# Kernel tuning notes

Hardware: AMD Instinct MI355X
Metric: run time of the kernel (lower is better)

The kernel has to match this reference:

```python
import jax, jax.numpy as jnp
import numpy as np

B, D, NT, NZ = 16384, 64, 128, 2048


def setup_inputs() -> dict:
    key = jax.random.key(0)
    ks = jax.random.split(key, 5)
    return {
        "t": jax.random.uniform(ks[0], (1,), dtype=jnp.float32),
        "z": jax.random.normal(ks[1], (B, D), dtype=jnp.float32),
        "logp_z": jnp.zeros((B, 1), jnp.float32),
        "centres_z": jax.random.normal(ks[2], (NZ, D), dtype=jnp.float32),
        "log_sigmas_z": jnp.zeros((NZ,), jnp.float32),
        "centres_t": jax.random.normal(ks[3], (NT, 1), dtype=jnp.float32),
        "log_sigmas_t": jnp.zeros((NT,), jnp.float32),
        "W": 0.01 * jax.random.normal(ks[4], (D, NT, NZ + 1), dtype=jnp.float32),
    }


def _gauss(r):
    return jnp.exp(-r * r)


def _forward(t, z, centres_z, log_sigmas_z, centres_t, log_sigmas_t, W):
    # time RBF features Phi_t: (NT,)
    r_t = jnp.abs(t.reshape(1, 1) - centres_t.reshape(1, -1)) / jnp.exp(log_sigmas_t)
    phi_t = _gauss(r_t).reshape(-1)
    W_t = jnp.einsum('dij,i->dj', W, phi_t)  # (D, NZ+1)
    Wz, bias = W_t[:, :-1], W_t[:, -1]       # bias comes from the appended ones column
    # z RBF features via squared-distance identity (avoids [B,NZ,D] blowup)
    sq = (jnp.sum(z * z, axis=1, keepdims=True)
          + jnp.sum(centres_z * centres_z, axis=1)[None, :]
          - 2.0 * z @ centres_z.T)
    sq = jnp.maximum(sq, 0.0)                 # (B, NZ) squared distances
    inv_s2 = jnp.exp(-2.0 * log_sigmas_z)     # 1/sigma_j^2, (NZ,)
    phi_z = jnp.exp(-sq * inv_s2)             # gaussian(||z-c_j||/s_j), (B, NZ)
    dz_dt = phi_z @ Wz.T + bias               # (B, D)
    # exact Jacobian trace for gaussian basis:
    #   d phi_j / d z_i = -2 * phi_j * (z_i - c_{j,i}) / s_j^2
    #   tr(J)_b = sum_j phi_{b,j} * inv_s2_j * (-2) * (sum_i Wz[i,j] z_{b,i} - sum_i Wz[i,j] c_{j,i})
    q = jnp.einsum('dj,jd->j', Wz, centres_z)  # (NZ,)
    trace = -2.0 * jnp.sum(phi_z * inv_s2 * (z @ Wz - q), axis=1)  # (B,)
    dlogp_z_dt = -trace[:, None]               # (B, 1)
    return dz_dt, dlogp_z_dt


def reference(t, z, logp_z, centres_z, log_sigmas_z, centres_t, log_sigmas_t, W):
    return _forward(t, z, centres_z, log_sigmas_z, centres_t, log_sigmas_t, W)
```

## Files before the change

kernel.cpp:

```cpp
#include <hip/hip_runtime.h>
#include <math.h>

typedef unsigned int uint;
typedef unsigned short ushort;
typedef __attribute__((ext_vector_type(8))) short short8;
typedef __attribute__((ext_vector_type(4))) float f32x4;

#define BB  16384
#define DD  64
#define NT_ 128
#define NZ_ 2048
#define NJ_ 2049

#define BIAS_OFF 0
#define Q_OFF    64
#define CC_OFF   2112
#define INV_OFF  4160
#define ZB_OFF   6208
#define CZB_OFF  530496
#define WZTB_OFF 596032
#define WZB_OFF  661568

__device__ __forceinline__ ushort f2b(float x) {
  uint u = __float_as_uint(x);
  uint r = (u + 0x7FFFu + ((u >> 16) & 1u)) >> 16;
  return (ushort)r;
}
__device__ __forceinline__ float b2f(ushort h) {
  return __uint_as_float(((uint)h) << 16);
}

__global__ __launch_bounds__(256) void k_wt(
    const float* __restrict__ t, const float* __restrict__ ct,
    const float* __restrict__ lst, const float* __restrict__ W,
    ushort* __restrict__ wzb, float* __restrict__ bias)
{
  __shared__ float ph[NT_];
  int tx = threadIdx.x;
  float t0 = t[0];
  if (tx < NT_) {
    float r = fabsf(t0 - ct[tx]) * __expf(-lst[tx]);
    ph[tx] = __expf(-r * r);
  }
  __syncthreads();
  int d = blockIdx.y;
  int j = blockIdx.x * 256 + tx;
  if (j >= NJ_) return;
  const float* Wp = W + (size_t)d * NT_ * NJ_ + j;
  float acc = 0.f;
#pragma unroll 16
  for (int i = 0; i < NT_; ++i) acc += Wp[(size_t)i * NJ_] * ph[i];
  if (j < NZ_) wzb[d * NZ_ + j] = f2b(acc);
  else         bias[d] = acc;
}

__global__ __launch_bounds__(256) void k_prep(
    const float* __restrict__ cz, const float* __restrict__ lsz,
    const ushort* __restrict__ wzb,
    float* __restrict__ q, float* __restrict__ cc, float* __restrict__ inv,
    ushort* __restrict__ czb, ushort* __restrict__ wztb)
{
  __shared__ ushort wt[64][72];
  int tid = threadIdx.x;
  int cb0 = blockIdx.x * 64;
#pragma unroll
  for (int k = 0; k < 2; ++k) {
    int f = k * 256 + tid;
    int d = f >> 3, s = f & 7;
    *(short8*)&wt[d][s * 8] = *(const short8*)(wzb + (size_t)d * NZ_ + cb0 + s * 8);
  }
  __syncthreads();
  int c_l = tid >> 2, part = tid & 3;
  int c = cb0 + c_l;
  float qa = 0.f, ca = 0.f;
  ushort czl[16];
  const float4* cz4 = (const float4*)(cz + (size_t)c * DD + part * 16);
#pragma unroll
  for (int x = 0; x < 4; ++x) {
    float4 v = cz4[x];
    float va[4] = {v.x, v.y, v.z, v.w};
#pragma unroll
    for (int k = 0; k < 4; ++k) {
      int d = part * 16 + x * 4 + k;
      ca += va[k] * va[k];
      qa += b2f(wt[d][c_l]) * va[k];
      czl[x * 4 + k] = f2b(va[k]);
    }
  }
  {
    short8 o0, o1;
#pragma unroll
    for (int k = 0; k < 8; ++k) { o0[k] = (short)czl[k]; o1[k] = (short)czl[8 + k]; }
    *(short8*)(czb + (size_t)c * DD + part * 16)     = o0;
    *(short8*)(czb + (size_t)c * DD + part * 16 + 8) = o1;
  }
  {
    short8 o0, o1;
#pragma unroll
    for (int k = 0; k < 8; ++k) {
      o0[k] = (short)wt[part * 16 + k][c_l];
      o1[k] = (short)wt[part * 16 + 8 + k][c_l];
    }
    *(short8*)(wztb + (size_t)c * DD + part * 16)     = o0;
    *(short8*)(wztb + (size_t)c * DD + part * 16 + 8) = o1;
  }
  qa += __shfl_xor(qa, 1); qa += __shfl_xor(qa, 2);
  ca += __shfl_xor(ca, 1); ca += __shfl_xor(ca, 2);
  if (part == 0) {
    q[c]  = qa;
    cc[c] = ca;
    inv[c] = __expf(-2.f * lsz[c]);
  }
}

__global__ __launch_bounds__(256) void k_zb(
    const float* __restrict__ z, ushort* __restrict__ zb)
{
  int f = blockIdx.x * 256 + threadIdx.x;
  const float4* z4 = (const float4*)z;
  float4 v0 = z4[f * 2], v1 = z4[f * 2 + 1];
  short8 o;
  o[0] = (short)f2b(v0.x); o[1] = (short)f2b(v0.y);
  o[2] = (short)f2b(v0.z); o[3] = (short)f2b(v0.w);
  o[4] = (short)f2b(v1.x); o[5] = (short)f2b(v1.y);
  o[6] = (short)f2b(v1.z); o[7] = (short)f2b(v1.w);
  *(short8*)(zb + (size_t)f * 8) = o;
}

#define KC 32

__global__ __launch_bounds__(512) void k_fused(
    const ushort* __restrict__ zb,
    const ushort* __restrict__ czb,
    const ushort* __restrict__ wztb,
    const ushort* __restrict__ wzb,
    const float* __restrict__ qg, const float* __restrict__ ccg,
    const float* __restrict__ invg, const float* __restrict__ bias,
    float* __restrict__ out)
{
  __shared__ float qs[NZ_], ccs[NZ_], invs[NZ_];
  __shared__ ushort phs[8][2][16][40];
  __shared__ float eps[64][68];
  __shared__ float dlr[4][64];

  int tid  = threadIdx.x;
  int wv   = tid >> 6, lane = tid & 63;
  int lrow = lane & 15, quad = lane >> 4;
  int ws = wv >> 1;
  int h  = wv & 1;
  int b0 = blockIdx.x * 64;

#pragma unroll
  for (int k = 0; k < 4; ++k) {
    int idx = k * 512 + tid;
    qs[idx] = qg[idx]; ccs[idx] = ccg[idx]; invs[idx] = invg[idx];
  }

  short8 a[2][2];
#pragma unroll
  for (int mt = 0; mt < 2; ++mt) {
    const ushort* zr = zb + (size_t)(b0 + h * 32 + mt * 16 + lrow) * DD;
    a[mt][0] = *(const short8*)(zr + quad * 8);
    a[mt][1] = *(const short8*)(zr + 32 + quad * 8);
  }
  float zzr[2][4];
#pragma unroll
  for (int mt = 0; mt < 2; ++mt) {
    float p = 0.f;
#pragma unroll
    for (int k = 0; k < 8; ++k) {
      float v0 = b2f((ushort)a[mt][0][k]), v1 = b2f((ushort)a[mt][1][k]);
      p += v0 * v0 + v1 * v1;
    }
    p += __shfl_xor(p, 16);
    p += __shfl_xor(p, 32);
#pragma unroll
    for (int i = 0; i < 4; ++i) zzr[mt][i] = __shfl(p, quad * 4 + i);
  }
  __syncthreads();

  f32x4 acc[2][4];
#pragma unroll
  for (int mt = 0; mt < 2; ++mt)
#pragma unroll
    for (int nt = 0; nt < 4; ++nt) acc[mt][nt] = (f32x4){0.f, 0.f, 0.f, 0.f};
  float dl[2][4] = {{0.f}};

  const f32x4 zero = (f32x4){0.f, 0.f, 0.f, 0.f};
  int cbase = ws * 512;
  for (int cc0 = 0; cc0 < 512; cc0 += KC) {
    int c0 = cbase + cc0;
#pragma unroll
    for (int nt = 0; nt < 2; ++nt) {
      const ushort* cr = czb  + (size_t)(c0 + nt * 16 + lrow) * DD;
      const ushort* wr = wztb + (size_t)(c0 + nt * 16 + lrow) * DD;
      short8 bc0 = *(const short8*)(cr + quad * 8);
      short8 bc1 = *(const short8*)(cr + 32 + quad * 8);
      short8 bw0 = *(const short8*)(wr + quad * 8);
      short8 bw1 = *(const short8*)(wr + 32 + quad * 8);
      int cl = nt * 16 + lrow, cg = c0 + cl;
      float ccv = ccs[cg], iv = invs[cg], qv = qs[cg];
#pragma unroll
      for (int mt = 0; mt < 2; ++mt) {
        f32x4 d1 = __builtin_amdgcn_mfma_f32_16x16x32_bf16(a[mt][0], bc0, zero, 0, 0, 0);
        d1       = __builtin_amdgcn_mfma_f32_16x16x32_bf16(a[mt][1], bc1, d1,   0, 0, 0);
        f32x4 d2 = __builtin_amdgcn_mfma_f32_16x16x32_bf16(a[mt][0], bw0, zero, 0, 0, 0);
        d2       = __builtin_amdgcn_mfma_f32_16x16x32_bf16(a[mt][1], bw1, d2,   0, 0, 0);
#pragma unroll
        for (int i = 0; i < 4; ++i) {
          float s = zzr[mt][i] + ccv - 2.f * d1[i];
          s = fmaxf(s, 0.f);
          float p = __expf(-s * iv);
          dl[mt][i] += p * iv * (d2[i] - qv);
          phs[wv][mt][quad * 4 + i][cl] = f2b(p);
        }
      }
    }
    short8 ap0 = *(const short8*)&phs[wv][0][lrow][quad * 8];
    short8 ap1 = *(const short8*)&phs[wv][1][lrow][quad * 8];
#pragma unroll
    for (int nt = 0; nt < 4; ++nt) {
      short8 bb = *(const short8*)(wzb + (size_t)(nt * 16 + lrow) * NZ_ + c0 + quad * 8);
      acc[0][nt] = __builtin_amdgcn_mfma_f32_16x16x32_bf16(ap0, bb, acc[0][nt], 0, 0, 0);
      acc[1][nt] = __builtin_amdgcn_mfma_f32_16x16x32_bf16(ap1, bb, acc[1][nt], 0, 0, 0);
    }
  }

#pragma unroll
  for (int mt = 0; mt < 2; ++mt)
#pragma unroll
    for (int i = 0; i < 4; ++i) {
      float v = dl[mt][i];
      v += __shfl_xor(v, 1);
      v += __shfl_xor(v, 2);
      v += __shfl_xor(v, 4);
      v += __shfl_xor(v, 8);
      if (lrow == 0) dlr[ws][h * 32 + mt * 16 + quad * 4 + i] = v;
    }

  for (int s = 0; s < 4; ++s) {
    __syncthreads();
    if (ws == s) {
#pragma unroll
      for (int mt = 0; mt < 2; ++mt)
#pragma unroll
        for (int nt = 0; nt < 4; ++nt)
#pragma unroll
          for (int i = 0; i < 4; ++i) {
            int r = h * 32 + mt * 16 + quad * 4 + i;
            int d = nt * 16 + lrow;
            if (s == 0) eps[r][d] = acc[mt][nt][i];
            else        eps[r][d] += acc[mt][nt][i];
          }
    }
  }
  __syncthreads();

  {
    int r = tid >> 3, d0 = (tid & 7) * 8;
    float4 e0 = *(const float4*)&eps[r][d0];
    float4 e1 = *(const float4*)&eps[r][d0 + 4];
    float4 bv0 = *(const float4*)&bias[d0];
    float4 bv1 = *(const float4*)&bias[d0 + 4];
    float4 o0, o1;
    o0.x = e0.x + bv0.x; o0.y = e0.y + bv0.y; o0.z = e0.z + bv0.z; o0.w = e0.w + bv0.w;
    o1.x = e1.x + bv1.x; o1.y = e1.y + bv1.y; o1.z = e1.z + bv1.z; o1.w = e1.w + bv1.w;
    *(float4*)&out[(size_t)(b0 + r) * DD + d0]     = o0;
    *(float4*)&out[(size_t)(b0 + r) * DD + d0 + 4] = o1;
  }
  if (tid < 64) {
    float s = dlr[0][tid] + dlr[1][tid] + dlr[2][tid] + dlr[3][tid];
    out[(size_t)BB * DD + b0 + tid] = 2.f * s;
  }
}

extern "C" void kernel_launch(void* const* d_in, const int* in_sizes, int n_in,
                              void* d_out, int out_size, void* d_ws, size_t ws_size,
                              hipStream_t stream)
{
  const float* t   = (const float*)d_in[0];
  const float* z   = (const float*)d_in[1];
  const float* cz  = (const float*)d_in[3];
  const float* lsz = (const float*)d_in[4];
  const float* ct  = (const float*)d_in[5];
  const float* lst = (const float*)d_in[6];
  const float* W   = (const float*)d_in[7];
  float* out = (float*)d_out;
  float* ws  = (float*)d_ws;

  float*  bias = ws + BIAS_OFF;
  float*  q    = ws + Q_OFF;
  float*  cc   = ws + CC_OFF;
  float*  inv  = ws + INV_OFF;
  ushort* zbp  = (ushort*)(ws + ZB_OFF);
  ushort* czb  = (ushort*)(ws + CZB_OFF);
  ushort* wztb = (ushort*)(ws + WZTB_OFF);
  ushort* wzb  = (ushort*)(ws + WZB_OFF);

  k_wt<<<dim3(9, 64), 256, 0, stream>>>(t, ct, lst, W, wzb, bias);
  k_prep<<<dim3(32), 256, 0, stream>>>(cz, lsz, wzb, q, cc, inv, czb, wztb);
  k_zb<<<dim3(512), 256, 0, stream>>>(z, zbp);
  k_fused<<<dim3(BB / 64), 512, 0, stream>>>(zbp, czb, wztb, wzb, q, cc, inv, bias, out);
}
```

Measured before the change: 165.0 us.

## Split W contraction over time-RBF chunks and shrink fused kernel LDS footprint

The W-by-phi_t contraction is split into four chunks of 32 time centres across a third grid dimension. Each chunk writes float partials, and the prep kernel sums them and also produces the bf16 Wz, its transpose and the bias. The goal is more parallelism when streaming the large W tensor. In the fused kernel the per-centre q/cc/inv tables are no longer staged in shared memory and are read from global memory instead. The phi and epilogue buffers now share one aliased LDS region, with launch bounds requesting more resident blocks. This trades extra partial-sum traffic and global scalar loads for higher occupancy.

```diff
diff --git a/kernel.cpp b/kernel.cpp
--- a/kernel.cpp
+++ b/kernel.cpp
@@ -20,6 +20,7 @@
 #define CZB_OFF  530496
 #define WZTB_OFF 596032
 #define WZB_OFF  661568
+#define PART_OFF 727104
 
 __device__ __forceinline__ ushort f2b(float x) {
   uint u = __float_as_uint(x);
@@ -30,60 +31,70 @@
   return __uint_as_float(((uint)h) << 16);
 }
 
-__global__ __launch_bounds__(256) void k_wt(
+__global__ __launch_bounds__(256) void k_wt1(
     const float* __restrict__ t, const float* __restrict__ ct,
     const float* __restrict__ lst, const float* __restrict__ W,
-    ushort* __restrict__ wzb, float* __restrict__ bias)
-{
-  __shared__ float ph[NT_];
+    float* __restrict__ part)
+{
+  __shared__ float ph[32];
   int tx = threadIdx.x;
-  float t0 = t[0];
-  if (tx < NT_) {
-    float r = fabsf(t0 - ct[tx]) * __expf(-lst[tx]);
+  int d  = blockIdx.y;
+  int ic = blockIdx.z;
+  if (tx < 32) {
+    int i = ic * 32 + tx;
+    float r = fabsf(t[0] - ct[i]) * __expf(-lst[i]);
     ph[tx] = __expf(-r * r);
   }
   __syncthreads();
-  int d = blockIdx.y;
   int j = blockIdx.x * 256 + tx;
   if (j >= NJ_) return;
-  const float* Wp = W + (size_t)d * NT_ * NJ_ + j;
+  const float* Wp = W + (size_t)d * NT_ * NJ_ + (size_t)(ic * 32) * NJ_ + j;
   float acc = 0.f;
-#pragma unroll 16
-  for (int i = 0; i < NT_; ++i) acc += Wp[(size_t)i * NJ_] * ph[i];
-  if (j < NZ_) wzb[d * NZ_ + j] = f2b(acc);
-  else         bias[d] = acc;
+#pragma unroll
+  for (int k = 0; k < 32; ++k) acc += Wp[(size_t)k * NJ_] * ph[k];
+  part[((size_t)ic * 64 + d) * NJ_ + j] = acc;
 }
 
 __global__ __launch_bounds__(256) void k_prep(
-    const float* __restrict__ cz, const float* __restrict__ lsz,
-    const ushort* __restrict__ wzb,
+    const float* __restrict__ part, const float* __restrict__ cz,
+    const float* __restrict__ lsz,
     float* __restrict__ q, float* __restrict__ cc, float* __restrict__ inv,
-    ushort* __restrict__ czb, ushort* __restrict__ wztb)
-{
-  __shared__ ushort wt[64][72];
+    float* __restrict__ bias,
+    ushort* __restrict__ wzb, ushort* __restrict__ czb, ushort* __restrict__ wztb)
+{
+  __shared__ float wtf[64][65];
   int tid = threadIdx.x;
   int cb0 = blockIdx.x * 64;
 #pragma unroll
-  for (int k = 0; k < 2; ++k) {
+  for (int k = 0; k < 16; ++k) {
     int f = k * 256 + tid;
-    int d = f >> 3, s = f & 7;
-    *(short8*)&wt[d][s * 8] = *(const short8*)(wzb + (size_t)d * NZ_ + cb0 + s * 8);
+    int d = f >> 6, c = f & 63;
+    size_t idx = (size_t)d * NJ_ + cb0 + c;
+    float s = part[idx] + part[(size_t)64 * NJ_ + idx]
+            + part[(size_t)128 * NJ_ + idx] + part[(size_t)192 * NJ_ + idx];
+    wtf[d][c] = s;
+    wzb[(size_t)d * NZ_ + cb0 + c] = f2b(s);
+  }
+  if (blockIdx.x == 0 && tid < 64) {
+    size_t idx = (size_t)tid * NJ_ + 2048;
+    bias[tid] = part[idx] + part[(size_t)64 * NJ_ + idx]
+              + part[(size_t)128 * NJ_ + idx] + part[(size_t)192 * NJ_ + idx];
   }
   __syncthreads();
-  int c_l = tid >> 2, part = tid & 3;
+  int c_l = tid >> 2, part4 = tid & 3;
   int c = cb0 + c_l;
   float qa = 0.f, ca = 0.f;
   ushort czl[16];
-  const float4* cz4 = (const float4*)(cz + (size_t)c * DD + part * 16);
+  const float4* cz4 = (const float4*)(cz + (size_t)c * DD + part4 * 16);
 #pragma unroll
   for (int x = 0; x < 4; ++x) {
     float4 v = cz4[x];
     float va[4] = {v.x, v.y, v.z, v.w};
 #pragma unroll
     for (int k = 0; k < 4; ++k) {
-      int d = part * 16 + x * 4 + k;
+      int d = part4 * 16 + x * 4 + k;
       ca += va[k] * va[k];
-      qa += b2f(wt[d][c_l]) * va[k];
+      qa += wtf[d][c_l] * va[k];
       czl[x * 4 + k] = f2b(va[k]);
     }
   }
@@ -91,22 +102,22 @@
     short8 o0, o1;
 #pragma unroll
     for (int k = 0; k < 8; ++k) { o0[k] = (short)czl[k]; o1[k] = (short)czl[8 + k]; }
-    *(short8*)(czb + (size_t)c * DD + part * 16)     = o0;
-    *(short8*)(czb + (size_t)c * DD + part * 16 + 8) = o1;
+    *(short8*)(czb + (size_t)c * DD + part4 * 16)     = o0;
+    *(short8*)(czb + (size_t)c * DD + part4 * 16 + 8) = o1;
   }
   {
     short8 o0, o1;
 #pragma unroll
     for (int k = 0; k < 8; ++k) {
-      o0[k] = (short)wt[part * 16 + k][c_l];
-      o1[k] = (short)wt[part * 16 + 8 + k][c_l];
-    }
-    *(short8*)(wztb + (size_t)c * DD + part * 16)     = o0;
-    *(short8*)(wztb + (size_t)c * DD + part * 16 + 8) = o1;
+      o0[k] = (short)f2b(wtf[part4 * 16 + k][c_l]);
+      o1[k] = (short)f2b(wtf[part4 * 16 + 8 + k][c_l]);
+    }
+    *(short8*)(wztb + (size_t)c * DD + part4 * 16)     = o0;
+    *(short8*)(wztb + (size_t)c * DD + part4 * 16 + 8) = o1;
   }
   qa += __shfl_xor(qa, 1); qa += __shfl_xor(qa, 2);
   ca += __shfl_xor(ca, 1); ca += __shfl_xor(ca, 2);
-  if (part == 0) {
+  if (part4 == 0) {
     q[c]  = qa;
     cc[c] = ca;
     inv[c] = __expf(-2.f * lsz[c]);
@@ -128,8 +139,9 @@
 }
 
 #define KC 32
-
-__global__ __launch_bounds__(512) void k_fused(
+#define PH_LD 40
+
+__global__ __launch_bounds__(512, 6) void k_fused(
     const ushort* __restrict__ zb,
     const ushort* __restrict__ czb,
     const ushort* __restrict__ wztb,
@@ -138,10 +150,10 @@
     const float* __restrict__ invg, const float* __restrict__ bias,
     float* __restrict__ out)
 {
-  __shared__ float qs[NZ_], ccs[NZ_], invs[NZ_];
-  __shared__ ushort phs[8][2][16][40];
-  __shared__ float eps[64][68];
+  __shared__ char smem[20480];
   __shared__ float dlr[4][64];
+  ushort* phs = (ushort*)smem;
+  float*  eps = (float*)smem;
 
   int tid  = threadIdx.x;
   int wv   = tid >> 6, lane = tid & 63;
@@ -150,12 +162,6 @@
   int h  = wv & 1;
   int b0 = blockIdx.x * 64;
 
-#pragma unroll
-  for (int k = 0; k < 4; ++k) {
-    int idx = k * 512 + tid;
-    qs[idx] = qg[idx]; ccs[idx] = ccg[idx]; invs[idx] = invg[idx];
-  }
-
   short8 a[2][2];
 #pragma unroll
   for (int mt = 0; mt < 2; ++mt) {
@@ -177,7 +183,6 @@
 #pragma unroll
     for (int i = 0; i < 4; ++i) zzr[mt][i] = __shfl(p, quad * 4 + i);
   }
-  __syncthreads();
 
   f32x4 acc[2][4];
 #pragma unroll
@@ -188,18 +193,19 @@
 
   const f32x4 zero = (f32x4){0.f, 0.f, 0.f, 0.f};
   int cbase = ws * 512;
+  int pbase = (wv * 2) * 16 * PH_LD;
   for (int cc0 = 0; cc0 < 512; cc0 += KC) {
     int c0 = cbase + cc0;
 #pragma unroll
     for (int nt = 0; nt < 2; ++nt) {
-      const ushort* cr = czb  + (size_t)(c0 + nt * 16 + lrow) * DD;
-      const ushort* wr = wztb + (size_t)(c0 + nt * 16 + lrow) * DD;
+      int cl = nt * 16 + lrow, cg = c0 + cl;
+      const ushort* cr = czb  + (size_t)cg * DD;
+      const ushort* wr = wztb + (size_t)cg * DD;
       short8 bc0 = *(const short8*)(cr + quad * 8);
       short8 bc1 = *(const short8*)(cr + 32 + quad * 8);
       short8 bw0 = *(const short8*)(wr + quad * 8);
       short8 bw1 = *(const short8*)(wr + 32 + quad * 8);
-      int cl = nt * 16 + lrow, cg = c0 + cl;
-      float ccv = ccs[cg], iv = invs[cg], qv = qs[cg];
+      float ccv = ccg[cg], iv = invg[cg], qv = qg[cg];
 #pragma unroll
       for (int mt = 0; mt < 2; ++mt) {
         f32x4 d1 = __builtin_amdgcn_mfma_f32_16x16x32_bf16(a[mt][0], bc0, zero, 0, 0, 0);
@@ -212,12 +218,12 @@
           s = fmaxf(s, 0.f);
           float p = __expf(-s * iv);
           dl[mt][i] += p * iv * (d2[i] - qv);
-          phs[wv][mt][quad * 4 + i][cl] = f2b(p);
+          phs[pbase + (mt * 16 + quad * 4 + i) * PH_LD + cl] = f2b(p);
         }
       }
     }
-    short8 ap0 = *(const short8*)&phs[wv][0][lrow][quad * 8];
-    short8 ap1 = *(const short8*)&phs[wv][1][lrow][quad * 8];
+    short8 ap0 = *(const short8*)&phs[pbase + lrow * PH_LD + quad * 8];
+    short8 ap1 = *(const short8*)&phs[pbase + (16 + lrow) * PH_LD + quad * 8];
 #pragma unroll
     for (int nt = 0; nt < 4; ++nt) {
       short8 bb = *(const short8*)(wzb + (size_t)(nt * 16 + lrow) * NZ_ + c0 + quad * 8);
@@ -249,8 +255,8 @@
           for (int i = 0; i < 4; ++i) {
             int r = h * 32 + mt * 16 + quad * 4 + i;
             int d = nt * 16 + lrow;
-            if (s == 0) eps[r][d] = acc[mt][nt][i];
-            else        eps[r][d] += acc[mt][nt][i];
+            if (s == 0) eps[r * 68 + d] = acc[mt][nt][i];
+            else        eps[r * 68 + d] += acc[mt][nt][i];
           }
     }
   }
@@ -258,8 +264,8 @@
 
   {
     int r = tid >> 3, d0 = (tid & 7) * 8;
-    float4 e0 = *(const float4*)&eps[r][d0];
-    float4 e1 = *(const float4*)&eps[r][d0 + 4];
+    float4 e0 = *(const float4*)&eps[r * 68 + d0];
+    float4 e1 = *(const float4*)&eps[r * 68 + d0 + 4];
     float4 bv0 = *(const float4*)&bias[d0];
     float4 bv1 = *(const float4*)&bias[d0 + 4];
     float4 o0, o1;
@@ -296,9 +302,10 @@
   ushort* czb  = (ushort*)(ws + CZB_OFF);
   ushort* wztb = (ushort*)(ws + WZTB_OFF);
   ushort* wzb  = (ushort*)(ws + WZB_OFF);
-
-  k_wt<<<dim3(9, 64), 256, 0, stream>>>(t, ct, lst, W, wzb, bias);
-  k_prep<<<dim3(32), 256, 0, stream>>>(cz, lsz, wzb, q, cc, inv, czb, wztb);
+  float*  part = ws + PART_OFF;
+
+  k_wt1<<<dim3(9, 64, 4), 256, 0, stream>>>(t, ct, lst, W, part);
+  k_prep<<<dim3(32), 256, 0, stream>>>(part, cz, lsz, q, cc, inv, bias, wzb, czb, wztb);
   k_zb<<<dim3(512), 256, 0, stream>>>(z, zbp);
   k_fused<<<dim3(BB / 64), 512, 0, stream>>>(zbp, czb, wztb, wzb, q, cc, inv, bias, out);
 }
```

Measured after the change: 277.2 us. 68.0% more time.
